# Performance work log

Hardware: AMD Instinct MI355X
Metric: run time of the kernel (lower is better)

## Reference

```python
import jax, jax.numpy as jnp
import numpy as np

N, E = 20000, 320000          # nodes, edges (avg in-degree ~16)
F_IN, EMB, T, OUT = 40, 40, 5, 2
F_T = EMB // T                # per-tower output width = 8
EPS_STD, EPS_GN = 1e-5, 1e-5


def _lin_init(k, fan_in, fan_out, extra=()):
    return jax.random.normal(k, (*extra, fan_in, fan_out), jnp.float32) / np.sqrt(fan_in)


def setup_inputs() -> dict:
    key = jax.random.key(0)
    ks = jax.random.split(key, 8)
    # deg histogram in init: all 20000 nodes with degree 16 -> avg_deg['log'] = log(16+1)
    return dict(
        x=jax.random.normal(ks[0], (N, F_IN), jnp.float32),
        edge_index=jax.random.randint(ks[1], (2, E), 0, N),
        W_pre=_lin_init(ks[2], 2 * F_IN, F_IN, (T,)),   # per-tower pre-MLP
        b_pre=jnp.zeros((T, F_IN), jnp.float32),
        W_post=_lin_init(ks[3], 13 * F_IN, F_T, (T,)),  # (4 agg * 3 scalers + 1 residual) * F_in
        b_post=jnp.zeros((T, F_T), jnp.float32),
        W_lin=_lin_init(ks[4], T * F_T, EMB),           # PNAConv final mixing linear
        b_lin=jnp.zeros((EMB,), jnp.float32),
        gn_weight=jnp.ones((EMB,), jnp.float32),
        gn_bias=jnp.zeros((EMB,), jnp.float32),
        gn_mean_scale=jnp.ones((EMB,), jnp.float32),
        W1=_lin_init(ks[5], EMB, EMB),                  # head hidden linear
        b1=jnp.zeros((EMB,), jnp.float32),
        W2=_lin_init(ks[6], EMB, OUT),                  # head output linear
        b2=jnp.zeros((OUT,), jnp.float32),
        avg_deg_log=jnp.float32(np.log(17.0)),
    )


def _pna_conv(x, src, dst, W_pre, b_pre, W_post, b_post, W_lin, b_lin, avg_deg_log):
    xi, xj = x[dst], x[src]                              # gather: [E, F]
    h = jnp.concatenate([xi, xj], axis=-1)               # [E, 2F]
    m = jnp.einsum('ef,tfg->etg', h, W_pre) + b_pre      # per-tower messages [E, T, F]
    cnt = jax.ops.segment_sum(jnp.ones((E,), m.dtype), dst, num_segments=N)  # in-degree [N]
    denom = jnp.maximum(cnt, 1.0)[:, None, None]
    mean = jax.ops.segment_sum(m, dst, num_segments=N) / denom
    mean2 = jax.ops.segment_sum(m * m, dst, num_segments=N) / denom
    std = jnp.sqrt(jax.nn.relu(mean2 - mean * mean) + EPS_STD)
    has = (cnt > 0)[:, None, None]
    mn = jnp.where(has, jax.ops.segment_min(m, dst, num_segments=N), 0.0)
    mx = jnp.where(has, jax.ops.segment_max(m, dst, num_segments=N), 0.0)
    agg = jnp.concatenate([mean, mn, mx, std], axis=-1)  # [N, T, 4F]
    deg = jnp.maximum(cnt, 1.0)[:, None, None]
    logd = jnp.log(deg + 1.0)
    out = jnp.concatenate(
        [agg, agg * (logd / avg_deg_log), agg * (avg_deg_log / logd)], axis=-1)  # [N, T, 12F]
    out = jnp.concatenate(
        [jnp.broadcast_to(x[:, None, :], (N, T, x.shape[-1])), out], axis=-1)    # [N, T, 13F]
    out = jnp.einsum('ntf,tfg->ntg', out, W_post) + b_post                       # [N, T, F_T]
    return out.reshape(N, T * F_T) @ W_lin + b_lin


def _graph_norm(x, w, b, mean_scale):
    mean = jnp.mean(x, axis=0, keepdims=True)
    out = x - mean_scale * mean
    var = jnp.mean(out * out, axis=0, keepdims=True)
    return w * out / jnp.sqrt(var + EPS_GN) + b


def reference(x, edge_index, W_pre, b_pre, W_post, b_post, W_lin, b_lin,
              gn_weight, gn_bias, gn_mean_scale, W1, b1, W2, b2, avg_deg_log):
    src, dst = edge_index[0], edge_index[1]
    h = _pna_conv(x, src, dst, W_pre, b_pre, W_post, b_post, W_lin, b_lin, avg_deg_log)
    h = jax.nn.relu(_graph_norm(h, gn_weight, gn_bias, gn_mean_scale))
    h = jax.nn.relu(h @ W1 + b1)   # dropout_rate=None -> no dropout
    return h @ W2 + b2
```

## Files before the change

kernel.cpp:

```cpp
#include <hip/hip_runtime.h>
#include <math.h>

#define N_NODES 20000
#define N_EDGES 320000
#define F_IN 40
#define T_TOW 5
#define EMB 40
#define NPB_PRE 16
#define NBLK_PM 313
#define ECHUNK 16
#define STRIDE 64

typedef __attribute__((ext_vector_type(8))) _Float16 half8;
typedef __attribute__((ext_vector_type(2))) _Float16 half2_t;
typedef __attribute__((ext_vector_type(4))) float f32x4;

#define WS_BAR     0
#define WS_CURSOR  320
#define WS_SSRC    80384
#define WS_MS      5200384
#define WS_MD      13200384
#define WS_AGG     21200384
#define WS_XPOST   53200384
#define WS_H0T     69200384
#define WS_PART    72400384

__global__ __launch_bounds__(256) void k_pre(const float* __restrict__ x,
                                             const float* __restrict__ W_pre,
                                             const float* __restrict__ b_pre,
                                             const float* __restrict__ W_post,
                                             const float* __restrict__ b_post,
                                             _Float16* __restrict__ mS,
                                             _Float16* __restrict__ mD,
                                             float* __restrict__ xpostT,
                                             int* __restrict__ cursor,
                                             int* __restrict__ bar) {
  const int tid = threadIdx.x;
  const int n0 = blockIdx.x * NPB_PRE;
  if (blockIdx.x == 0 && tid == 0) *bar = 0;
  if (tid < NPB_PRE) cursor[n0 + tid] = (n0 + tid) * STRIDE;
  const bool statlane = tid < 200;
  const int q = tid - 200;
  const bool xplane = (q >= 0 && q < 40);
  const int tc = statlane ? tid : 199;
  const int t = tc / 40, g = tc - t * 40;
  const int t2 = xplane ? q / 8 : 0, g2 = xplane ? q - (q / 8) * 8 : 0;
  float wA[40], wB[40];
  const float* Wt = W_pre + t * 3200;
#pragma unroll
  for (int j = 0; j < 40; ++j) {
    wA[j] = statlane ? Wt[j * 40 + g] : W_post[t2 * 4160 + j * 8 + g2];
    wB[j] = statlane ? Wt[(40 + j) * 40 + g] : 0.f;
  }
  const float bias = statlane ? b_pre[t * 40 + g] : b_post[t2 * 8 + g2];
  for (int ni = 0; ni < NPB_PRE; ++ni) {
    const int n = n0 + ni;
    const float* xr = x + n * F_IN;
    float aA = bias, aB = 0.f;
#pragma unroll
    for (int j = 0; j < 40; j += 4) {
      const float4 xv = *(const float4*)(xr + j);
      aA += xv.x * wA[j] + xv.y * wA[j + 1] + xv.z * wA[j + 2] + xv.w * wA[j + 3];
      aB += xv.x * wB[j] + xv.y * wB[j + 1] + xv.z * wB[j + 2] + xv.w * wB[j + 3];
    }
    if (statlane) {
      mD[n * 200 + tc] = (_Float16)aA;
      mS[n * 200 + tc] = (_Float16)aB;
    } else if (xplane) {
      xpostT[t2 * (N_NODES * 8) + n * 8 + g2] = aA;
    }
  }
}

__global__ __launch_bounds__(256) void k_scatter(const int* __restrict__ src,
                                                 const int* __restrict__ dst,
                                                 int* __restrict__ cursor,
                                                 int* __restrict__ ssrc) {
  int i = blockIdx.x * 256 + threadIdx.x;
  if (i < N_EDGES) {
    int d = dst[i];
    int pos = atomicAdd(&cursor[d], 1);
    ssrc[pos] = src[i];
  }
}

__global__ __launch_bounds__(256) void k_edge(const _Float16* __restrict__ mS,
                                              const _Float16* __restrict__ mD,
                                              const int* __restrict__ cursor,
                                              const int* __restrict__ ssrc,
                                              _Float16* __restrict__ aggS) {
  const int lane = threadIdx.x & 63;
  const int wv = threadIdx.x >> 6;
  const int n = blockIdx.x * 4 + wv;
  const int r0 = n * STRIDE;
  const int r1 = __builtin_amdgcn_readfirstlane(cursor[n]);
  const int cnt = r1 - r0;
  const int cpa = lane;
  const bool bact = lane < 36;
  const int cpb = bact ? 64 + lane : 99;
  const half2_t mda = ((const half2_t*)(mD + n * 200))[cpa];
  const half2_t mdb = ((const half2_t*)(mD + n * 200))[cpb];

  const _Float16 HINF = (_Float16)65504.f;
  half2_t suma = {0, 0}, ssqa = {0, 0}, sumb = {0, 0}, ssqb = {0, 0};
  half2_t mna = {HINF, HINF}, mxa = {-HINF, -HINF};
  half2_t mnb = {HINF, HINF}, mxb = {-HINF, -HINF};
  half2_t va = {0, 0}, vb = {0, 0};

  if (cnt > 0) {
    for (int p = r0; p < r1; p += ECHUNK) {
      half2_t ha[ECHUNK], hb[ECHUNK];
#pragma unroll
      for (int i = 0; i < ECHUNK; ++i) {
        const int qe = (p + i < r1) ? (p + i) : (r1 - 1);
        const int s = __builtin_amdgcn_readfirstlane(ssrc[qe]);
        const half2_t* row = (const half2_t*)(mS + s * 200);
        ha[i] = row[cpa];
        hb[i] = row[cpb];
      }
#pragma unroll
      for (int i = 0; i < ECHUNK; ++i) {
        suma += ha[i];
        ssqa += ha[i] * ha[i];
        mna = __builtin_elementwise_min(mna, ha[i]);
        mxa = __builtin_elementwise_max(mxa, ha[i]);
        sumb += hb[i];
        ssqb += hb[i] * hb[i];
        mnb = __builtin_elementwise_min(mnb, hb[i]);
        mxb = __builtin_elementwise_max(mxb, hb[i]);
      }
      va = ha[ECHUNK - 1];
      vb = hb[ECHUNK - 1];
    }
  }

  const int padded = ((cnt + ECHUNK - 1) / ECHUNK) * ECHUNK;
  const float d = (float)(padded - cnt);
  const float inv = (cnt > 0) ? 1.f / (float)cnt : 0.f;
#pragma unroll
  for (int set = 0; set < 2; ++set) {
    if (set == 1 && !bact) break;
    const int cp = set == 0 ? cpa : cpb;
    const half2_t sum2 = set == 0 ? suma : sumb;
    const half2_t ssq2 = set == 0 ? ssqa : ssqb;
    const half2_t mn2 = set == 0 ? mna : mnb;
    const half2_t mx2 = set == 0 ? mxa : mxb;
    const half2_t vl2 = set == 0 ? va : vb;
    const half2_t md2 = set == 0 ? mda : mdb;
    half2_t omean, omn, omx, osd;
#pragma unroll
    for (int j = 0; j < 2; ++j) {
      float mean, mnf, mxf, sd;
      if (cnt > 0) {
        const float vl = (float)vl2[j];
        const float sf = (float)sum2[j] - d * vl;
        const float qf = (float)ssq2[j] - d * vl * vl;
        const float msm = sf * inv;
        const float var = qf * inv - msm * msm;
        sd = sqrtf(fmaxf(var, 0.f) + 1e-5f);
        const float mdf = (float)md2[j];
        mean = mdf + msm;
        mnf = mdf + (float)mn2[j];
        mxf = mdf + (float)mx2[j];
      } else {
        mean = 0.f; mnf = 0.f; mxf = 0.f; sd = sqrtf(1e-5f);
      }
      omean[j] = (_Float16)mean;
      omn[j] = (_Float16)mnf;
      omx[j] = (_Float16)mxf;
      osd[j] = (_Float16)sd;
    }
    const int t = cp / 20, g = 2 * (cp - t * 20);
    _Float16* abase = aggS + ((size_t)t * N_NODES + n) * 160 + g;
    *(half2_t*)(abase) = omean;
    *(half2_t*)(abase + 40) = omn;
    *(half2_t*)(abase + 80) = omx;
    *(half2_t*)(abase + 120) = osd;
  }
}

__global__ __launch_bounds__(320, 3) void k_back(const _Float16* __restrict__ aggT,
                                                 const int* __restrict__ cursor,
                                                 const float* __restrict__ W_post,
                                                 const float* __restrict__ avg_dl,
                                                 const float* __restrict__ xpostT,
                                                 const float* __restrict__ W_lin,
                                                 const float* __restrict__ b_lin,
                                                 float* __restrict__ h0T,
                                                 float* __restrict__ partial,
                                                 int* __restrict__ bar,
                                                 const float* __restrict__ gn_w,
                                                 const float* __restrict__ gn_b,
                                                 const float* __restrict__ gn_ms,
                                                 const float* __restrict__ W1,
                                                 const float* __restrict__ b1,
                                                 const float* __restrict__ W2,
                                                 const float* __restrict__ b2,
                                                 float* __restrict__ out) {
  __shared__ float sA[64 * 41];
  __shared__ float sH[64 * 41];
  __shared__ float sSp[4][80];
  const int tid = threadIdx.x;
  const int t = tid >> 6;
  const int l = tid & 63;
  const int n0 = blockIdx.x * 64;
  const int c = l & 15;
  const int kg = l >> 4;

  const float* Wt = W_post + t * 4160;
  half8 b1f[5], b2f[5];
#pragma unroll
  for (int ks = 0; ks < 5; ++ks) {
#pragma unroll
    for (int j = 0; j < 8; ++j) {
      const int k = ks * 32 + kg * 8 + j;
      const float w1v = (c < 8) ? Wt[(40 + k) * 8 + c] : Wt[(200 + k) * 8 + (c - 8)];
      const float w2v = (c < 8) ? Wt[(360 + k) * 8 + c] : 0.f;
      b1f[ks][j] = (_Float16)w1v;
      b2f[ks][j] = (_Float16)w2v;
    }
  }
  const float avg = avg_dl[0];

  for (int tile = 0; tile < 4; ++tile) {
    const int nb = n0 + tile * 16;
    int nA = nb + c;
    if (nA >= N_NODES) nA = N_NODES - 1;
    const half8* ar = (const half8*)(aggT + ((size_t)t * N_NODES + nA) * 160);
    half8 af[5];
#pragma unroll
    for (int ks = 0; ks < 5; ++ks) af[ks] = ar[ks * 4 + kg];
    f32x4 acc1 = {0.f, 0.f, 0.f, 0.f}, acc2 = {0.f, 0.f, 0.f, 0.f};
#pragma unroll
    for (int ks = 0; ks < 5; ++ks) {
      acc1 = __builtin_amdgcn_mfma_f32_16x16x32_f16(af[ks], b1f[ks], acc1, 0, 0, 0);
      acc2 = __builtin_amdgcn_mfma_f32_16x16x32_f16(af[ks], b2f[ks], acc2, 0, 0, 0);
    }
    float bp[4];
#pragma unroll
    for (int r = 0; r < 4; ++r) bp[r] = __shfl_xor(acc1[r], 8, 64);
    if (c < 8) {
#pragma unroll
      for (int r = 0; r < 4; ++r) {
        const int nn0 = nb + kg * 4 + r;
        const int nn = (nn0 < N_NODES) ? nn0 : N_NODES - 1;
        const int cnt = cursor[nn] - nn * STRIDE;
        const float ld = logf(fmaxf((float)cnt, 1.f) + 1.f);
        const float s1 = ld / avg, s2 = avg / ld;
        const float xp = xpostT[t * (N_NODES * 8) + nn * 8 + c];
        sA[(tile * 16 + kg * 4 + r) * 41 + t * 8 + c] =
            acc1[r] + s1 * bp[r] + s2 * acc2[r] + xp;
      }
    }
  }
  __syncthreads();

  {
    const int c0 = t * 8;
    float acc[8];
#pragma unroll
    for (int j = 0; j < 8; ++j) acc[j] = b_lin[c0 + j];
    for (int k = 0; k < 40; ++k) {
      const float p = sA[l * 41 + k];
      const float* w = W_lin + k * EMB + c0;
#pragma unroll
      for (int j = 0; j < 8; ++j) acc[j] = fmaf(p, w[j], acc[j]);
    }
    const int n = n0 + l;
    const bool ok = n < N_NODES;
    if (ok) {
#pragma unroll
      for (int j = 0; j < 8; ++j) h0T[(c0 + j) * N_NODES + n] = acc[j];
    }
#pragma unroll
    for (int j = 0; j < 8; ++j) {
      float sv = ok ? acc[j] : 0.f;
      float qv = sv * sv;
#pragma unroll
      for (int m = 32; m >= 1; m >>= 1) {
        sv += __shfl_xor(sv, m, 64);
        qv += __shfl_xor(qv, m, 64);
      }
      if (l == 0) {
        partial[blockIdx.x * 80 + c0 + j] = sv;
        partial[blockIdx.x * 80 + 40 + c0 + j] = qv;
      }
    }
  }

  __syncthreads();
  if (tid == 0) {
    __threadfence();
    atomicAdd(bar, 1);
    while (__hip_atomic_load(bar, __ATOMIC_ACQUIRE, __HIP_MEMORY_SCOPE_AGENT)
           < NBLK_PM) {
      __builtin_amdgcn_s_sleep(8);
    }
  }
  __syncthreads();

  {
    const int part_i = tid / 80;
    const int col = tid - part_i * 80;
    float a0 = 0.f, a1 = 0.f, a2 = 0.f, a3 = 0.f;
    int b = part_i;
    for (; b + 12 < NBLK_PM; b += 16) {
      a0 += partial[b * 80 + col];
      a1 += partial[(b + 4) * 80 + col];
      a2 += partial[(b + 8) * 80 + col];
      a3 += partial[(b + 12) * 80 + col];
    }
    for (; b < NBLK_PM; b += 4) a0 += partial[b * 80 + col];
    sSp[part_i][col] = (a0 + a1) + (a2 + a3);
  }
  __syncthreads();

  const float invN = 1.f / (float)N_NODES;
  for (int i = 0; i < 8; ++i) {
    const int idx = tid + i * 320;
    const int e = idx >> 6, r = idx & 63;
    const int nn0 = n0 + r;
    const int nn = (nn0 < N_NODES) ? nn0 : 0;
    const float S1e = sSp[0][e] + sSp[1][e] + sSp[2][e] + sSp[3][e];
    const float S2e = sSp[0][40 + e] + sSp[1][40 + e] + sSp[2][40 + e] + sSp[3][40 + e];
    const float M = S1e * invN;
    const float ms = gn_ms[e];
    const float var = S2e * invN - ms * (2.f - ms) * M * M;
    const float sc = gn_w[e] / sqrtf(var + 1e-5f);
    const float he = h0T[e * N_NODES + nn];
    sA[r * 41 + e] = fmaxf((he - ms * M) * sc + gn_b[e], 0.f);
  }
  __syncthreads();
  {
    const int c0 = t * 8;
    float acc[8];
#pragma unroll
    for (int j = 0; j < 8; ++j) acc[j] = b1[c0 + j];
    for (int k = 0; k < 40; ++k) {
      const float p = sA[l * 41 + k];
      const float* w = W1 + k * EMB + c0;
#pragma unroll
      for (int j = 0; j < 8; ++j) acc[j] = fmaf(p, w[j], acc[j]);
    }
#pragma unroll
    for (int j = 0; j < 8; ++j) sH[l * 41 + c0 + j] = fmaxf(acc[j], 0.f);
  }
  __syncthreads();
  if (tid < 64) {
    const int n = n0 + tid;
    if (n < N_NODES) {
      float o0 = b2[0], o1 = b2[1];
      const float* hr = sH + tid * 41;
#pragma unroll
      for (int k = 0; k < 40; ++k) {
        const float r = hr[k];
        o0 = fmaf(r, W2[k * 2], o0);
        o1 = fmaf(r, W2[k * 2 + 1], o1);
      }
      out[n * 2] = o0;
      out[n * 2 + 1] = o1;
    }
  }
}

extern "C" void kernel_launch(void* const* d_in, const int* in_sizes, int n_in,
                              void* d_out, int out_size, void* d_ws, size_t ws_size,
                              hipStream_t stream) {
  const float* x      = (const float*)d_in[0];
  const int*   ei     = (const int*)d_in[1];
  const float* W_pre  = (const float*)d_in[2];
  const float* b_pre  = (const float*)d_in[3];
  const float* W_post = (const float*)d_in[4];
  const float* b_post = (const float*)d_in[5];
  const float* W_lin  = (const float*)d_in[6];
  const float* b_lin  = (const float*)d_in[7];
  const float* gn_w   = (const float*)d_in[8];
  const float* gn_b   = (const float*)d_in[9];
  const float* gn_ms  = (const float*)d_in[10];
  const float* W1     = (const float*)d_in[11];
  const float* b1     = (const float*)d_in[12];
  const float* W2     = (const float*)d_in[13];
  const float* b2     = (const float*)d_in[14];
  const float* avg_dl = (const float*)d_in[15];
  float* out = (float*)d_out;

  char* ws = (char*)d_ws;
  int* bar    = (int*)(ws + WS_BAR);
  int* cursor = (int*)(ws + WS_CURSOR);
  int* ssrc   = (int*)(ws + WS_SSRC);
  _Float16* mS   = (_Float16*)(ws + WS_MS);
  _Float16* mD   = (_Float16*)(ws + WS_MD);
  _Float16* aggS = (_Float16*)(ws + WS_AGG);
  float* xpostT  = (float*)(ws + WS_XPOST);
  float* h0T     = (float*)(ws + WS_H0T);
  float* part    = (float*)(ws + WS_PART);
  const int* e_src = ei;
  const int* e_dst = ei + N_EDGES;

  k_pre<<<N_NODES / NPB_PRE, 256, 0, stream>>>(x, W_pre, b_pre, W_post, b_post,
                                               mS, mD, xpostT, cursor, bar);
  k_scatter<<<(N_EDGES + 255) / 256, 256, 0, stream>>>(e_src, e_dst, cursor, ssrc);
  k_edge<<<N_NODES / 4, 256, 0, stream>>>(mS, mD, cursor, ssrc, aggS);
  k_back<<<NBLK_PM, 320, 0, stream>>>(aggS, cursor, W_post, avg_dl, xpostT,
                                      W_lin, b_lin, h0T, part, bar,
                                      gn_w, gn_b, gn_ms, W1, b1, W2, b2, out);
}
```

Baseline: 225.7 us.

## Fuse scatter, edge aggregation and post-MLP into one persistent kernel

Merges the scatter, edge-aggregation and back-end kernels into a single persistent kernel of 250 blocks of 80 nodes each, separated by two software grid barriers. Each block aggregates the nodes it later consumes, so the h0T global round trip is kept in shared memory. Source indices are loaded once per wave and broadcast with readlane instead of a scalar load per edge. This removes two launches and global traffic, but cuts edge-phase parallelism to 1000 waves. It also relies on all 250 blocks being co-resident for the spin barriers.

```diff
diff --git a/kernel.cpp b/kernel.cpp
--- a/kernel.cpp
+++ b/kernel.cpp
@@ -7,7 +7,8 @@
 #define T_TOW 5
 #define EMB 40
 #define NPB_PRE 16
-#define NBLK_PM 313
+#define NBLK_MEGA 250
+#define NPB 80
 #define ECHUNK 16
 #define STRIDE 64
 
@@ -22,7 +23,6 @@
 #define WS_MD      13200384
 #define WS_AGG     21200384
 #define WS_XPOST   53200384
-#define WS_H0T     69200384
 #define WS_PART    72400384
 
 __global__ __launch_bounds__(256) void k_pre(const float* __restrict__ x,
@@ -72,294 +72,305 @@
   }
 }
 
-__global__ __launch_bounds__(256) void k_scatter(const int* __restrict__ src,
-                                                 const int* __restrict__ dst,
-                                                 int* __restrict__ cursor,
-                                                 int* __restrict__ ssrc) {
-  int i = blockIdx.x * 256 + threadIdx.x;
-  if (i < N_EDGES) {
-    int d = dst[i];
-    int pos = atomicAdd(&cursor[d], 1);
-    ssrc[pos] = src[i];
-  }
-}
-
-__global__ __launch_bounds__(256) void k_edge(const _Float16* __restrict__ mS,
-                                              const _Float16* __restrict__ mD,
-                                              const int* __restrict__ cursor,
-                                              const int* __restrict__ ssrc,
-                                              _Float16* __restrict__ aggS) {
-  const int lane = threadIdx.x & 63;
-  const int wv = threadIdx.x >> 6;
-  const int n = blockIdx.x * 4 + wv;
-  const int r0 = n * STRIDE;
-  const int r1 = __builtin_amdgcn_readfirstlane(cursor[n]);
-  const int cnt = r1 - r0;
-  const int cpa = lane;
-  const bool bact = lane < 36;
-  const int cpb = bact ? 64 + lane : 99;
-  const half2_t mda = ((const half2_t*)(mD + n * 200))[cpa];
-  const half2_t mdb = ((const half2_t*)(mD + n * 200))[cpb];
-
-  const _Float16 HINF = (_Float16)65504.f;
-  half2_t suma = {0, 0}, ssqa = {0, 0}, sumb = {0, 0}, ssqb = {0, 0};
-  half2_t mna = {HINF, HINF}, mxa = {-HINF, -HINF};
-  half2_t mnb = {HINF, HINF}, mxb = {-HINF, -HINF};
-  half2_t va = {0, 0}, vb = {0, 0};
-
-  if (cnt > 0) {
-    for (int p = r0; p < r1; p += ECHUNK) {
-      half2_t ha[ECHUNK], hb[ECHUNK];
-#pragma unroll
-      for (int i = 0; i < ECHUNK; ++i) {
-        const int qe = (p + i < r1) ? (p + i) : (r1 - 1);
-        const int s = __builtin_amdgcn_readfirstlane(ssrc[qe]);
-        const half2_t* row = (const half2_t*)(mS + s * 200);
-        ha[i] = row[cpa];
-        hb[i] = row[cpb];
-      }
-#pragma unroll
-      for (int i = 0; i < ECHUNK; ++i) {
-        suma += ha[i];
-        ssqa += ha[i] * ha[i];
-        mna = __builtin_elementwise_min(mna, ha[i]);
-        mxa = __builtin_elementwise_max(mxa, ha[i]);
-        sumb += hb[i];
-        ssqb += hb[i] * hb[i];
-        mnb = __builtin_elementwise_min(mnb, hb[i]);
-        mxb = __builtin_elementwise_max(mxb, hb[i]);
-      }
-      va = ha[ECHUNK - 1];
-      vb = hb[ECHUNK - 1];
-    }
-  }
-
-  const int padded = ((cnt + ECHUNK - 1) / ECHUNK) * ECHUNK;
-  const float d = (float)(padded - cnt);
-  const float inv = (cnt > 0) ? 1.f / (float)cnt : 0.f;
-#pragma unroll
-  for (int set = 0; set < 2; ++set) {
-    if (set == 1 && !bact) break;
-    const int cp = set == 0 ? cpa : cpb;
-    const half2_t sum2 = set == 0 ? suma : sumb;
-    const half2_t ssq2 = set == 0 ? ssqa : ssqb;
-    const half2_t mn2 = set == 0 ? mna : mnb;
-    const half2_t mx2 = set == 0 ? mxa : mxb;
-    const half2_t vl2 = set == 0 ? va : vb;
-    const half2_t md2 = set == 0 ? mda : mdb;
-    half2_t omean, omn, omx, osd;
-#pragma unroll
-    for (int j = 0; j < 2; ++j) {
-      float mean, mnf, mxf, sd;
-      if (cnt > 0) {
-        const float vl = (float)vl2[j];
-        const float sf = (float)sum2[j] - d * vl;
-        const float qf = (float)ssq2[j] - d * vl * vl;
-        const float msm = sf * inv;
-        const float var = qf * inv - msm * msm;
-        sd = sqrtf(fmaxf(var, 0.f) + 1e-5f);
-        const float mdf = (float)md2[j];
-        mean = mdf + msm;
-        mnf = mdf + (float)mn2[j];
-        mxf = mdf + (float)mx2[j];
-      } else {
-        mean = 0.f; mnf = 0.f; mxf = 0.f; sd = sqrtf(1e-5f);
-      }
-      omean[j] = (_Float16)mean;
-      omn[j] = (_Float16)mnf;
-      omx[j] = (_Float16)mxf;
-      osd[j] = (_Float16)sd;
-    }
-    const int t = cp / 20, g = 2 * (cp - t * 20);
-    _Float16* abase = aggS + ((size_t)t * N_NODES + n) * 160 + g;
-    *(half2_t*)(abase) = omean;
-    *(half2_t*)(abase + 40) = omn;
-    *(half2_t*)(abase + 80) = omx;
-    *(half2_t*)(abase + 120) = osd;
-  }
-}
-
-__global__ __launch_bounds__(320, 3) void k_back(const _Float16* __restrict__ aggT,
-                                                 const int* __restrict__ cursor,
-                                                 const float* __restrict__ W_post,
-                                                 const float* __restrict__ avg_dl,
-                                                 const float* __restrict__ xpostT,
-                                                 const float* __restrict__ W_lin,
-                                                 const float* __restrict__ b_lin,
-                                                 float* __restrict__ h0T,
-                                                 float* __restrict__ partial,
-                                                 int* __restrict__ bar,
-                                                 const float* __restrict__ gn_w,
-                                                 const float* __restrict__ gn_b,
-                                                 const float* __restrict__ gn_ms,
-                                                 const float* __restrict__ W1,
-                                                 const float* __restrict__ b1,
-                                                 const float* __restrict__ W2,
-                                                 const float* __restrict__ b2,
-                                                 float* __restrict__ out) {
-  __shared__ float sA[64 * 41];
-  __shared__ float sH[64 * 41];
-  __shared__ float sSp[4][80];
-  const int tid = threadIdx.x;
-  const int t = tid >> 6;
-  const int l = tid & 63;
-  const int n0 = blockIdx.x * 64;
-  const int c = l & 15;
-  const int kg = l >> 4;
-
-  const float* Wt = W_post + t * 4160;
-  half8 b1f[5], b2f[5];
-#pragma unroll
-  for (int ks = 0; ks < 5; ++ks) {
-#pragma unroll
-    for (int j = 0; j < 8; ++j) {
-      const int k = ks * 32 + kg * 8 + j;
-      const float w1v = (c < 8) ? Wt[(40 + k) * 8 + c] : Wt[(200 + k) * 8 + (c - 8)];
-      const float w2v = (c < 8) ? Wt[(360 + k) * 8 + c] : 0.f;
-      b1f[ks][j] = (_Float16)w1v;
-      b2f[ks][j] = (_Float16)w2v;
-    }
-  }
-  const float avg = avg_dl[0];
-
-  for (int tile = 0; tile < 4; ++tile) {
-    const int nb = n0 + tile * 16;
-    int nA = nb + c;
-    if (nA >= N_NODES) nA = N_NODES - 1;
-    const half8* ar = (const half8*)(aggT + ((size_t)t * N_NODES + nA) * 160);
-    half8 af[5];
-#pragma unroll
-    for (int ks = 0; ks < 5; ++ks) af[ks] = ar[ks * 4 + kg];
-    f32x4 acc1 = {0.f, 0.f, 0.f, 0.f}, acc2 = {0.f, 0.f, 0.f, 0.f};
-#pragma unroll
-    for (int ks = 0; ks < 5; ++ks) {
-      acc1 = __builtin_amdgcn_mfma_f32_16x16x32_f16(af[ks], b1f[ks], acc1, 0, 0, 0);
-      acc2 = __builtin_amdgcn_mfma_f32_16x16x32_f16(af[ks], b2f[ks], acc2, 0, 0, 0);
-    }
-    float bp[4];
-#pragma unroll
-    for (int r = 0; r < 4; ++r) bp[r] = __shfl_xor(acc1[r], 8, 64);
-    if (c < 8) {
-#pragma unroll
-      for (int r = 0; r < 4; ++r) {
-        const int nn0 = nb + kg * 4 + r;
-        const int nn = (nn0 < N_NODES) ? nn0 : N_NODES - 1;
-        const int cnt = cursor[nn] - nn * STRIDE;
-        const float ld = logf(fmaxf((float)cnt, 1.f) + 1.f);
-        const float s1 = ld / avg, s2 = avg / ld;
-        const float xp = xpostT[t * (N_NODES * 8) + nn * 8 + c];
-        sA[(tile * 16 + kg * 4 + r) * 41 + t * 8 + c] =
-            acc1[r] + s1 * bp[r] + s2 * acc2[r] + xp;
-      }
-    }
-  }
-  __syncthreads();
-
-  {
-    const int c0 = t * 8;
-    float acc[8];
-#pragma unroll
-    for (int j = 0; j < 8; ++j) acc[j] = b_lin[c0 + j];
-    for (int k = 0; k < 40; ++k) {
-      const float p = sA[l * 41 + k];
-      const float* w = W_lin + k * EMB + c0;
-#pragma unroll
-      for (int j = 0; j < 8; ++j) acc[j] = fmaf(p, w[j], acc[j]);
-    }
-    const int n = n0 + l;
-    const bool ok = n < N_NODES;
-    if (ok) {
-#pragma unroll
-      for (int j = 0; j < 8; ++j) h0T[(c0 + j) * N_NODES + n] = acc[j];
-    }
-#pragma unroll
-    for (int j = 0; j < 8; ++j) {
-      float sv = ok ? acc[j] : 0.f;
-      float qv = sv * sv;
-#pragma unroll
-      for (int m = 32; m >= 1; m >>= 1) {
-        sv += __shfl_xor(sv, m, 64);
-        qv += __shfl_xor(qv, m, 64);
-      }
-      if (l == 0) {
-        partial[blockIdx.x * 80 + c0 + j] = sv;
-        partial[blockIdx.x * 80 + 40 + c0 + j] = qv;
-      }
-    }
-  }
-
-  __syncthreads();
-  if (tid == 0) {
+__device__ __forceinline__ void grid_barrier(int* bar, int target) {
+  __syncthreads();
+  if (threadIdx.x == 0) {
     __threadfence();
     atomicAdd(bar, 1);
-    while (__hip_atomic_load(bar, __ATOMIC_ACQUIRE, __HIP_MEMORY_SCOPE_AGENT)
-           < NBLK_PM) {
-      __builtin_amdgcn_s_sleep(8);
-    }
-  }
-  __syncthreads();
+    while (__hip_atomic_load(bar, __ATOMIC_ACQUIRE,
+                             __HIP_MEMORY_SCOPE_AGENT) < target) {
+      __builtin_amdgcn_s_sleep(2);
+    }
+  }
+  __syncthreads();
+  __threadfence();
+}
+
+__global__ __launch_bounds__(256) void k_mega(
+    const int* __restrict__ src, const int* __restrict__ dst,
+    const _Float16* __restrict__ mS, const _Float16* __restrict__ mD,
+    int* __restrict__ cursor, int* __restrict__ ssrc,
+    _Float16* __restrict__ aggS,
+    const float* __restrict__ W_post, const float* __restrict__ avg_dl,
+    const float* __restrict__ xpostT,
+    const float* __restrict__ W_lin, const float* __restrict__ b_lin,
+    float* __restrict__ partial, int* __restrict__ bar,
+    const float* __restrict__ gn_w, const float* __restrict__ gn_b,
+    const float* __restrict__ gn_ms,
+    const float* __restrict__ W1, const float* __restrict__ b1,
+    const float* __restrict__ W2, const float* __restrict__ b2,
+    float* __restrict__ out) {
+  __shared__ float sP[NPB * 41];
+  __shared__ float sH0[NPB * 41];
+  __shared__ float sH[NPB * 41];
+  __shared__ float sSp[3][80];
+  const int tid = threadIdx.x;
+  const int blk = blockIdx.x;
+  const int wv = tid >> 6, l = tid & 63;
+  const int n0 = blk * NPB;
+
+#pragma unroll
+  for (int i = 0; i < 5; ++i) {
+    const int e = blk * 1280 + i * 256 + tid;
+    const int d = dst[e];
+    const int pos = atomicAdd(&cursor[d], 1);
+    ssrc[pos] = src[e];
+  }
+  grid_barrier(bar, NBLK_MEGA);
 
   {
-    const int part_i = tid / 80;
-    const int col = tid - part_i * 80;
+    const _Float16 HINF = (_Float16)65504.f;
+    for (int it = 0; it < 20; ++it) {
+      const int n = n0 + it * 4 + wv;
+      const int r0 = n * STRIDE;
+      const int r1 = __builtin_amdgcn_readfirstlane(cursor[n]);
+      const int cnt = r1 - r0;
+      const int myidx = ssrc[r0 + l];
+      const int cpa = l;
+      const bool bact = l < 36;
+      const int cpb = bact ? 64 + l : 99;
+      const half2_t mda = ((const half2_t*)(mD + n * 200))[cpa];
+      const half2_t mdb = ((const half2_t*)(mD + n * 200))[cpb];
+      half2_t suma = {0, 0}, ssqa = {0, 0}, sumb = {0, 0}, ssqb = {0, 0};
+      half2_t mna = {HINF, HINF}, mxa = {-HINF, -HINF};
+      half2_t mnb = {HINF, HINF}, mxb = {-HINF, -HINF};
+      half2_t va = {0, 0}, vb = {0, 0};
+      if (cnt > 0) {
+        for (int p = 0; p < cnt; p += ECHUNK) {
+          half2_t ha[ECHUNK], hb[ECHUNK];
+#pragma unroll
+          for (int i = 0; i < ECHUNK; ++i) {
+            const int ii = (p + i < cnt) ? (p + i) : (cnt - 1);
+            const int s = __builtin_amdgcn_readlane(myidx, ii);
+            const half2_t* row = (const half2_t*)(mS + s * 200);
+            ha[i] = row[cpa];
+            hb[i] = row[cpb];
+          }
+#pragma unroll
+          for (int i = 0; i < ECHUNK; ++i) {
+            suma += ha[i]; ssqa += ha[i] * ha[i];
+            mna = __builtin_elementwise_min(mna, ha[i]);
+            mxa = __builtin_elementwise_max(mxa, ha[i]);
+            sumb += hb[i]; ssqb += hb[i] * hb[i];
+            mnb = __builtin_elementwise_min(mnb, hb[i]);
+            mxb = __builtin_elementwise_max(mxb, hb[i]);
+          }
+          va = ha[ECHUNK - 1];
+          vb = hb[ECHUNK - 1];
+        }
+      }
+      const int padded = ((cnt + ECHUNK - 1) / ECHUNK) * ECHUNK;
+      const float dpad = (float)(padded - cnt);
+      const float inv = (cnt > 0) ? 1.f / (float)cnt : 0.f;
+#pragma unroll
+      for (int set = 0; set < 2; ++set) {
+        if (set == 1 && !bact) break;
+        const int cp = set == 0 ? cpa : cpb;
+        const half2_t sum2 = set == 0 ? suma : sumb;
+        const half2_t ssq2 = set == 0 ? ssqa : ssqb;
+        const half2_t mn2 = set == 0 ? mna : mnb;
+        const half2_t mx2 = set == 0 ? mxa : mxb;
+        const half2_t vl2 = set == 0 ? va : vb;
+        const half2_t md2 = set == 0 ? mda : mdb;
+        half2_t omean, omn, omx, osd;
+#pragma unroll
+        for (int j = 0; j < 2; ++j) {
+          float mean, mnf, mxf, sd;
+          if (cnt > 0) {
+            const float vl = (float)vl2[j];
+            const float sf = (float)sum2[j] - dpad * vl;
+            const float qf = (float)ssq2[j] - dpad * vl * vl;
+            const float msm = sf * inv;
+            const float var = qf * inv - msm * msm;
+            sd = sqrtf(fmaxf(var, 0.f) + 1e-5f);
+            const float mdf = (float)md2[j];
+            mean = mdf + msm;
+            mnf = mdf + (float)mn2[j];
+            mxf = mdf + (float)mx2[j];
+          } else {
+            mean = 0.f; mnf = 0.f; mxf = 0.f; sd = sqrtf(1e-5f);
+          }
+          omean[j] = (_Float16)mean;
+          omn[j] = (_Float16)mnf;
+          omx[j] = (_Float16)mxf;
+          osd[j] = (_Float16)sd;
+        }
+        const int tt = cp / 20, g = 2 * (cp - tt * 20);
+        _Float16* abase = aggS + ((size_t)tt * N_NODES + n) * 160 + g;
+        *(half2_t*)(abase) = omean;
+        *(half2_t*)(abase + 40) = omn;
+        *(half2_t*)(abase + 80) = omx;
+        *(half2_t*)(abase + 120) = osd;
+      }
+    }
+  }
+  __threadfence_block();
+  __syncthreads();
+
+  {
+    const int c = l & 15;
+    const int kg = l >> 4;
+    const float avg = avg_dl[0];
+    for (int t = wv; t < T_TOW; t += 4) {
+      const float* Wt = W_post + t * 4160;
+      half8 b1f[5], b2f[5];
+#pragma unroll
+      for (int ks = 0; ks < 5; ++ks) {
+#pragma unroll
+        for (int j = 0; j < 8; ++j) {
+          const int k = ks * 32 + kg * 8 + j;
+          const float w1v = (c < 8) ? Wt[(40 + k) * 8 + c] : Wt[(200 + k) * 8 + (c - 8)];
+          const float w2v = (c < 8) ? Wt[(360 + k) * 8 + c] : 0.f;
+          b1f[ks][j] = (_Float16)w1v;
+          b2f[ks][j] = (_Float16)w2v;
+        }
+      }
+      for (int tile = 0; tile < 5; ++tile) {
+        const int nb = n0 + tile * 16;
+        const int nA = nb + c;
+        const half8* ar = (const half8*)(aggS + ((size_t)t * N_NODES + nA) * 160);
+        half8 af[5];
+#pragma unroll
+        for (int ks = 0; ks < 5; ++ks) af[ks] = ar[ks * 4 + kg];
+        f32x4 acc1 = {0.f, 0.f, 0.f, 0.f}, acc2 = {0.f, 0.f, 0.f, 0.f};
+#pragma unroll
+        for (int ks = 0; ks < 5; ++ks) {
+          acc1 = __builtin_amdgcn_mfma_f32_16x16x32_f16(af[ks], b1f[ks], acc1, 0, 0, 0);
+          acc2 = __builtin_amdgcn_mfma_f32_16x16x32_f16(af[ks], b2f[ks], acc2, 0, 0, 0);
+        }
+        float bp[4];
+#pragma unroll
+        for (int r = 0; r < 4; ++r) bp[r] = __shfl_xor(acc1[r], 8, 64);
+        if (c < 8) {
+#pragma unroll
+          for (int r = 0; r < 4; ++r) {
+            const int nn = nb + kg * 4 + r;
+            const int cnt = cursor[nn] - nn * STRIDE;
+            const float ld = logf(fmaxf((float)cnt, 1.f) + 1.f);
+            const float s1 = ld / avg, s2 = avg / ld;
+            const float xp = xpostT[t * (N_NODES * 8) + nn * 8 + c];
+            sP[(tile * 16 + kg * 4 + r) * 41 + t * 8 + c] =
+                acc1[r] + s1 * bp[r] + s2 * acc2[r] + xp;
+          }
+        }
+      }
+    }
+  }
+  __syncthreads();
+
+  {
+    const int c0 = wv * 10;
+    float svj[10], qvj[10];
+#pragma unroll
+    for (int j = 0; j < 10; ++j) { svj[j] = 0.f; qvj[j] = 0.f; }
+    for (int pass = 0; pass < 2; ++pass) {
+      const int ln = pass * 64 + l;
+      const bool okn = ln < NPB;
+      float acc[10];
+#pragma unroll
+      for (int j = 0; j < 10; ++j) acc[j] = b_lin[c0 + j];
+      if (okn) {
+        for (int k = 0; k < 40; ++k) {
+          const float p = sP[ln * 41 + k];
+          const float* w = W_lin + k * EMB + c0;
+#pragma unroll
+          for (int j = 0; j < 10; ++j) acc[j] = fmaf(p, w[j], acc[j]);
+        }
+#pragma unroll
+        for (int j = 0; j < 10; ++j) sH0[ln * 41 + c0 + j] = acc[j];
+      }
+#pragma unroll
+      for (int j = 0; j < 10; ++j) {
+        const float v = okn ? acc[j] : 0.f;
+        svj[j] += v;
+        qvj[j] += v * v;
+      }
+    }
+#pragma unroll
+    for (int j = 0; j < 10; ++j) {
+#pragma unroll
+      for (int m = 32; m >= 1; m >>= 1) {
+        svj[j] += __shfl_xor(svj[j], m, 64);
+        qvj[j] += __shfl_xor(qvj[j], m, 64);
+      }
+      if (l == 0) {
+        partial[blk * 80 + c0 + j] = svj[j];
+        partial[blk * 80 + 40 + c0 + j] = qvj[j];
+      }
+    }
+  }
+  grid_barrier(bar, 2 * NBLK_MEGA);
+
+  if (tid < 240) {
+    const int chunk = tid / 80;
+    const int col = tid - chunk * 80;
+    const int b0 = chunk * 84;
+    const int b1 = (b0 + 84 < NBLK_MEGA) ? b0 + 84 : NBLK_MEGA;
     float a0 = 0.f, a1 = 0.f, a2 = 0.f, a3 = 0.f;
-    int b = part_i;
-    for (; b + 12 < NBLK_PM; b += 16) {
-      a0 += partial[b * 80 + col];
-      a1 += partial[(b + 4) * 80 + col];
-      a2 += partial[(b + 8) * 80 + col];
-      a3 += partial[(b + 12) * 80 + col];
-    }
-    for (; b < NBLK_PM; b += 4) a0 += partial[b * 80 + col];
-    sSp[part_i][col] = (a0 + a1) + (a2 + a3);
-  }
-  __syncthreads();
-
-  const float invN = 1.f / (float)N_NODES;
-  for (int i = 0; i < 8; ++i) {
-    const int idx = tid + i * 320;
-    const int e = idx >> 6, r = idx & 63;
-    const int nn0 = n0 + r;
-    const int nn = (nn0 < N_NODES) ? nn0 : 0;
-    const float S1e = sSp[0][e] + sSp[1][e] + sSp[2][e] + sSp[3][e];
-    const float S2e = sSp[0][40 + e] + sSp[1][40 + e] + sSp[2][40 + e] + sSp[3][40 + e];
-    const float M = S1e * invN;
-    const float ms = gn_ms[e];
-    const float var = S2e * invN - ms * (2.f - ms) * M * M;
-    const float sc = gn_w[e] / sqrtf(var + 1e-5f);
-    const float he = h0T[e * N_NODES + nn];
-    sA[r * 41 + e] = fmaxf((he - ms * M) * sc + gn_b[e], 0.f);
-  }
-  __syncthreads();
+    int b = b0;
+    for (; b + 4 <= b1; b += 4) {
+      a0 += partial[(b + 0) * 80 + col];
+      a1 += partial[(b + 1) * 80 + col];
+      a2 += partial[(b + 2) * 80 + col];
+      a3 += partial[(b + 3) * 80 + col];
+    }
+    for (; b < b1; ++b) a0 += partial[b * 80 + col];
+    sSp[chunk][col] = (a0 + a1) + (a2 + a3);
+  }
+  __syncthreads();
+
   {
-    const int c0 = t * 8;
-    float acc[8];
-#pragma unroll
-    for (int j = 0; j < 8; ++j) acc[j] = b1[c0 + j];
+    const float invN = 1.f / (float)N_NODES;
+    for (int i = 0; i < 13; ++i) {
+      const int idx = tid + i * 256;
+      if (idx < 3200) {
+        const int e = idx / 80, r = idx - e * 80;
+        const float S1e = sSp[0][e] + sSp[1][e] + sSp[2][e];
+        const float S2e = sSp[0][40 + e] + sSp[1][40 + e] + sSp[2][40 + e];
+        const float M = S1e * invN;
+        const float ms = gn_ms[e];
+        const float var = S2e * invN - ms * (2.f - ms) * M * M;
+        const float sc = gn_w[e] / sqrtf(var + 1e-5f);
+        const float he = sH0[r * 41 + e];
+        sH0[r * 41 + e] = fmaxf((he - ms * M) * sc + gn_b[e], 0.f);
+      }
+    }
+  }
+  __syncthreads();
+
+  {
+    const int c0 = wv * 10;
+    for (int pass = 0; pass < 2; ++pass) {
+      const int ln = pass * 64 + l;
+      if (ln < NPB) {
+        float acc[10];
+#pragma unroll
+        for (int j = 0; j < 10; ++j) acc[j] = b1[c0 + j];
+        for (int k = 0; k < 40; ++k) {
+          const float p = sH0[ln * 41 + k];
+          const float* w = W1 + k * EMB + c0;
+#pragma unroll
+          for (int j = 0; j < 10; ++j) acc[j] = fmaf(p, w[j], acc[j]);
+        }
+#pragma unroll
+        for (int j = 0; j < 10; ++j) sH[ln * 41 + c0 + j] = fmaxf(acc[j], 0.f);
+      }
+    }
+  }
+  __syncthreads();
+
+  if (tid < NPB) {
+    const int n = n0 + tid;
+    float o0 = b2[0], o1 = b2[1];
+    const float* hr = sH + tid * 41;
+#pragma unroll
     for (int k = 0; k < 40; ++k) {
-      const float p = sA[l * 41 + k];
-      const float* w = W1 + k * EMB + c0;
-#pragma unroll
-      for (int j = 0; j < 8; ++j) acc[j] = fmaf(p, w[j], acc[j]);
-    }
-#pragma unroll
-    for (int j = 0; j < 8; ++j) sH[l * 41 + c0 + j] = fmaxf(acc[j], 0.f);
-  }
-  __syncthreads();
-  if (tid < 64) {
-    const int n = n0 + tid;
-    if (n < N_NODES) {
-      float o0 = b2[0], o1 = b2[1];
-      const float* hr = sH + tid * 41;
-#pragma unroll
-      for (int k = 0; k < 40; ++k) {
-        const float r = hr[k];
-        o0 = fmaf(r, W2[k * 2], o0);
-        o1 = fmaf(r, W2[k * 2 + 1], o1);
-      }
-      out[n * 2] = o0;
-      out[n * 2 + 1] = o1;
-    }
+      const float r = hr[k];
+      o0 = fmaf(r, W2[k * 2], o0);
+      o1 = fmaf(r, W2[k * 2 + 1], o1);
+    }
+    out[n * 2] = o0;
+    out[n * 2 + 1] = o1;
   }
 }
 
@@ -392,16 +403,14 @@
   _Float16* mD   = (_Float16*)(ws + WS_MD);
   _Float16* aggS = (_Float16*)(ws + WS_AGG);
   float* xpostT  = (float*)(ws + WS_XPOST);
-  float* h0T     = (float*)(ws + WS_H0T);
   float* part    = (float*)(ws + WS_PART);
   const int* e_src = ei;
   const int* e_dst = ei + N_EDGES;
 
   k_pre<<<N_NODES / NPB_PRE, 256, 0, stream>>>(x, W_pre, b_pre, W_post, b_post,
                                                mS, mD, xpostT, cursor, bar);
-  k_scatter<<<(N_EDGES + 255) / 256, 256, 0, stream>>>(e_src, e_dst, cursor, ssrc);
-  k_edge<<<N_NODES / 4, 256, 0, stream>>>(mS, mD, cursor, ssrc, aggS);
-  k_back<<<NBLK_PM, 320, 0, stream>>>(aggS, cursor, W_post, avg_dl, xpostT,
-                                      W_lin, b_lin, h0T, part, bar,
-                                      gn_w, gn_b, gn_ms, W1, b1, W2, b2, out);
+  k_mega<<<NBLK_MEGA, 256, 0, stream>>>(e_src, e_dst, mS, mD, cursor, ssrc,
+                                        aggS, W_post, avg_dl, xpostT,
+                                        W_lin, b_lin, part, bar,
+                                        gn_w, gn_b, gn_ms, W1, b1, W2, b2, out);
 }
```

Result: slower. 308.2 us (+36.5%).
